# Kernel tuning notes

Measured on AMD Instinct MI355X. Metric: run time of the kernel, lower is better.

## Reference

```python
import jax, jax.numpy as jnp
import numpy as np

B, S, HID, H, D = 4, 1024, 2048, 16, 128
ROT = D // 2  # GLM 2D rotary: rotary dim is half the head dim (64)


def _rope_tables(seq_len, dim, base=10000.0):
    # dim = ROT; inv_freq over dim//2 frequencies, emb = cat(freqs, freqs)
    inv_freq = 1.0 / (base ** (jnp.arange(0, dim, 2, dtype=jnp.float32) / dim))
    t = jnp.arange(seq_len, dtype=jnp.float32)
    freqs = jnp.einsum('s,f->sf', t, inv_freq)          # [S, dim//2]
    emb = jnp.concatenate([freqs, freqs], axis=-1)       # [S, dim]
    return jnp.cos(emb), jnp.sin(emb)


def _rotate_half(x):
    x1, x2 = jnp.split(x, 2, axis=-1)
    return jnp.concatenate([-x2, x1], axis=-1)


def _apply_rope(x, cos, sin, pos_id):
    # x: [B,H,S,ROT]; pos_id: [B,S]; tables: [S,ROT]
    c = cos[pos_id][:, None, :, :]  # [B,1,S,ROT]
    s = sin[pos_id][:, None, :, :]
    return x * c + _rotate_half(x) * s


def setup_inputs() -> dict:
    key = jax.random.key(0)
    ks = jax.random.split(key, 12)
    w = 0.02
    inp = {
        'query': jax.random.normal(ks[0], (B, S, HID), jnp.float32),
        'key': jax.random.normal(ks[1], (B, S, HID), jnp.float32),
        'value': jax.random.normal(ks[2], (B, S, HID), jnp.float32),
        'mask': jnp.zeros((B, 1, S, S), jnp.float32),
        'position_bias': jax.random.normal(ks[3], (1, H, S, S), jnp.float32) * 0.1,
        'prev_attn': jax.random.normal(ks[4], (B, H, S, S), jnp.float32) * 0.1,
        'position_ids': jax.random.randint(ks[5], (B, 2, S), 0, S, jnp.int32),
        'Wq': jax.random.normal(ks[6], (HID, HID), jnp.float32) * w,
        'bq': jnp.zeros((HID,), jnp.float32),
        'Wk': jax.random.normal(ks[7], (HID, HID), jnp.float32) * w,
        'bk': jnp.zeros((HID,), jnp.float32),
        'Wv': jax.random.normal(ks[8], (HID, HID), jnp.float32) * w,
        'bv': jnp.zeros((HID,), jnp.float32),
        'Wo': jax.random.normal(ks[9], (HID, HID), jnp.float32) * w,
        'bo': jnp.zeros((HID,), jnp.float32),
    }
    return inp


def reference(query, key, value, mask, position_bias, prev_attn,
              Wq, bq, Wk, bk, Wv, bv, Wo, bo, position_ids):
    # QKV projections -> [B,H,S,D]
    def proj(x, W, b):
        return (x @ W.T + b).reshape(B, S, H, D).transpose(0, 2, 1, 3)
    q = proj(query, Wq, bq)
    k = proj(key, Wk, bk)
    v = proj(value, Wv, bv)

    # GLM 2D rotary: split head dim in halves, rope each with its own ids
    q1, q2 = jnp.split(q, 2, axis=-1)
    k1, k2 = jnp.split(k, 2, axis=-1)
    cos, sin = _rope_tables(S, ROT)
    pid = position_ids[:, 0, :]        # [B,S]
    bid = position_ids[:, 1, :]        # [B,S]
    q1 = _apply_rope(q1, cos, sin, pid)
    k1 = _apply_rope(k1, cos, sin, pid)
    q2 = _apply_rope(q2, cos, sin, bid)
    k2 = _apply_rope(k2, cos, sin, bid)
    q = jnp.concatenate([q1, q2], axis=-1)
    k = jnp.concatenate([k1, k2], axis=-1)

    scores = jnp.einsum('bhsd,bhtd->bhst', q, k)
    scores = scores + position_bias
    scores = scores / jnp.sqrt(jnp.float32(D))
    scores = scores + mask
    scores = scores + prev_attn          # residual attention accumulation
    prev_attn_out = scores
    probs = jax.nn.softmax(scores, axis=-1)
    ctx = jnp.einsum('bhst,bhtd->bhsd', probs, v)
    ctx = ctx.transpose(0, 2, 1, 3).reshape(B, S, HID)
    out = ctx @ Wo.T + bo
    return out, prev_attn_out
```

## Files before the change

kernel.cpp:

```cpp
#include <hip/hip_runtime.h>


#define B_  4
#define S_  1024
#define HID_ 2048
#define H_  16
#define D_  128
#define M_  (B_ * S_)
#define RSQRT_D 0.08838834764831845f

typedef _Float16 f16x8 __attribute__((ext_vector_type(8)));
typedef float f32x4 __attribute__((ext_vector_type(4)));

#define MFMA16(a, b, c) __builtin_amdgcn_mfma_f32_16x16x32_f16(a, b, c, 0, 0, 0)

__device__ __forceinline__ void gll16(const void* g, void* l) {
  __builtin_amdgcn_global_load_lds(
      (const __attribute__((address_space(1))) void*)g,
      (__attribute__((address_space(3))) void*)l, 16, 0, 0);
}

__global__ void rope_table_kernel(float* __restrict__ tcos, float* __restrict__ tsin) {
  int i = blockIdx.x * blockDim.x + threadIdx.x;
  int pos = i >> 5, j = i & 31;
  float inv = expf(-(float)j * (9.210340371976184f / 32.0f));
  float ang = (float)pos * inv;
  tcos[i] = cosf(ang);
  tsin[i] = sinf(ang);
}

__global__ void cvt_kernel(const float* __restrict__ in, _Float16* __restrict__ out, int n8) {
  int i = blockIdx.x * blockDim.x + threadIdx.x;
  if (i >= n8) return;
  const float4* in4 = (const float4*)in;
  float4 a = in4[i * 2], b = in4[i * 2 + 1];
  f16x8 v;
  v[0] = (_Float16)a.x; v[1] = (_Float16)a.y; v[2] = (_Float16)a.z; v[3] = (_Float16)a.w;
  v[4] = (_Float16)b.x; v[5] = (_Float16)b.y; v[6] = (_Float16)b.z; v[7] = (_Float16)b.w;
  *(f16x8*)(out + (size_t)i * 8) = v;
}

template <int MODE>
__global__ __launch_bounds__(256) void proj_kernel(
    const _Float16* __restrict__ A, const _Float16* __restrict__ Bw,
    const float* __restrict__ bias, void* __restrict__ outp,
    const int* __restrict__ pids, const float* __restrict__ tcos,
    const float* __restrict__ tsin) {
  constexpr int N = HID_, K = HID_;
  constexpr int BK = 64;
  __shared__ _Float16 As[128 * BK];
  __shared__ _Float16 Bs[128 * BK];

  const int tid = threadIdx.x;
  const int bid = (blockIdx.x & 7) * 64 + (blockIdx.x >> 3);
  const int tm = bid >> 4, tn = bid & 15;
  const int m0 = tm * 128, n0 = tn * 128;
  const int w = tid >> 6, l = tid & 63;
  const int mw = (w >> 1) * 64, nw = (w & 1) * 64;
  const int lr = l & 15, lh = l >> 4;

  f32x4 acc[4][4] = {};

  for (int kt = 0; kt < K / BK; ++kt) {
    const int k0 = kt * BK;
    __syncthreads();
#pragma unroll
    for (int i = 0; i < 4; ++i) {
      const int e = i * 2048 + tid * 8;
      gll16(A + (size_t)(m0 + (e >> 6)) * K + k0 + (e & 63), As + e);
      gll16(Bw + (size_t)(n0 + (e >> 6)) * K + k0 + (e & 63), Bs + e);
    }
    asm volatile("s_waitcnt vmcnt(0)" ::: "memory");
    __syncthreads();
#pragma unroll
    for (int kk = 0; kk < 2; ++kk) {
      f16x8 af[4], bf[4];
#pragma unroll
      for (int mi = 0; mi < 4; ++mi)
        af[mi] = *(const f16x8*)(As + (mw + mi * 16 + lr) * BK + kk * 32 + lh * 8);
#pragma unroll
      for (int ni = 0; ni < 4; ++ni)
        bf[ni] = *(const f16x8*)(Bs + (nw + ni * 16 + lr) * BK + kk * 32 + lh * 8);
#pragma unroll
      for (int mi = 0; mi < 4; ++mi)
#pragma unroll
        for (int ni = 0; ni < 4; ++ni)
          acc[mi][ni] = MFMA16(af[mi], bf[ni], acc[mi][ni]);
    }
  }

  if constexpr (MODE == 2) {
    float* out = (float*)outp;
#pragma unroll
    for (int mi = 0; mi < 4; ++mi)
#pragma unroll
      for (int ni = 0; ni < 4; ++ni) {
        const int col = n0 + nw + ni * 16 + lr;
        const float bb = bias[col];
#pragma unroll
        for (int r = 0; r < 4; ++r) {
          const int row = m0 + mw + mi * 16 + lh * 4 + r;
          out[(size_t)row * N + col] = acc[mi][ni][r] + bb;
        }
      }
  } else if constexpr (MODE == 1) {
    _Float16* out = (_Float16*)outp;
#pragma unroll
    for (int mi = 0; mi < 4; ++mi)
#pragma unroll
      for (int ni = 0; ni < 4; ++ni) {
        const int col = n0 + nw + ni * 16 + lr;
        const float bb = bias[col];
        const int h = col >> 7, hd = col & 127;
#pragma unroll
        for (int r = 0; r < 4; ++r) {
          const int row = m0 + mw + mi * 16 + lh * 4 + r;
          const int b = row >> 10, s = row & 1023;
          out[(((size_t)(b * H_ + h)) * S_ + s) * D_ + hd] = (_Float16)(acc[mi][ni][r] + bb);
        }
      }
  } else {
    _Float16* out = (_Float16*)outp;
    const int sel = (nw >> 6) & 1;
#pragma unroll
    for (int mi = 0; mi < 4; ++mi) {
#pragma unroll
      for (int r = 0; r < 4; ++r) {
        const int row = m0 + mw + mi * 16 + lh * 4 + r;
        const int b = row >> 10, s = row & 1023;
        const int pos = pids[b * 2 * S_ + sel * S_ + s];
#pragma unroll
        for (int ni = 0; ni < 2; ++ni) {
          const int col = n0 + nw + ni * 16 + lr;
          const int j = ni * 16 + lr;
          const float c = tcos[pos * 32 + j];
          const float sn = tsin[pos * 32 + j];
          const float x1 = acc[mi][ni][r] + bias[col];
          const float x2 = acc[mi][ni + 2][r] + bias[col + 32];
          const int h = col >> 7, hd = col & 127;
          const size_t base = (((size_t)(b * H_ + h)) * S_ + s) * D_;
          out[base + hd] = (_Float16)(x1 * c - x2 * sn);
          out[base + hd + 32] = (_Float16)(x2 * c + x1 * sn);
        }
      }
    }
  }
}

__global__ __launch_bounds__(256) void transpose_kernel(const _Float16* __restrict__ in,
                                                        _Float16* __restrict__ out) {
  __shared__ _Float16 tile[32][33];
  const int plane = blockIdx.z;
  const int d0 = blockIdx.x * 32, s0 = blockIdx.y * 32;
  const int tx = threadIdx.x & 31, ty = threadIdx.x >> 5;
  const _Float16* ip = in + (size_t)plane * S_ * D_;
  _Float16* op = out + (size_t)plane * S_ * D_;
#pragma unroll
  for (int i = 0; i < 4; ++i)
    tile[ty + i * 8][tx] = ip[(size_t)(s0 + ty + i * 8) * D_ + d0 + tx];
  __syncthreads();
#pragma unroll
  for (int i = 0; i < 4; ++i)
    op[(size_t)(d0 + ty + i * 8) * S_ + s0 + tx] = tile[tx][ty + i * 8];
}

__global__ __launch_bounds__(256) void flash_kernel(
    const _Float16* __restrict__ q, const _Float16* __restrict__ k,
    const _Float16* __restrict__ vt, const float* __restrict__ pbias,
    const float* __restrict__ maskp, const float* __restrict__ prev,
    float* __restrict__ scores, _Float16* __restrict__ ctx) {
  constexpr int BT = 64;
  __shared__ _Float16 Ks[BT * D_];
  __shared__ _Float16 VTs[D_ * BT];
  __shared__ _Float16 Ps[4][16 * BT];

  const int tid = threadIdx.x, w = tid >> 6, l = tid & 63;
  const int lr = l & 15, lh = l >> 4;
  const int byh = blockIdx.y;
  const int b = byh >> 4, h = byh & 15;
  const size_t plane = (size_t)byh;
  const int q0 = blockIdx.x * 64 + w * 16;

  f16x8 qa[4];
#pragma unroll
  for (int kk = 0; kk < 4; ++kk)
    qa[kk] = *(const f16x8*)(q + (plane * S_ + q0 + lr) * D_ + kk * 32 + lh * 8);

  f32x4 o[8] = {};
  float m_r[4], l_r[4];
#pragma unroll
  for (int r = 0; r < 4; ++r) { m_r[r] = -1e30f; l_r[r] = 0.0f; }

  for (int tt = 0; tt < S_ / BT; ++tt) {
    const int t0 = tt * BT;
    __syncthreads();
#pragma unroll
    for (int i = 0; i < 4; ++i) {
      const int e = i * 2048 + tid * 8;
      gll16(k + (plane * S_ + t0 + (e >> 7)) * D_ + (e & 127), Ks + e);
      gll16(vt + (plane * D_ + (e >> 6)) * S_ + t0 + (e & 63), VTs + e);
    }
    asm volatile("s_waitcnt vmcnt(0)" ::: "memory");
    __syncthreads();

    f32x4 sa[4] = {};
#pragma unroll
    for (int nt = 0; nt < 4; ++nt)
#pragma unroll
      for (int kk = 0; kk < 4; ++kk) {
        f16x8 kb = *(const f16x8*)(Ks + (nt * 16 + lr) * D_ + kk * 32 + lh * 8);
        sa[nt] = MFMA16(qa[kk], kb, sa[nt]);
      }

    float p[4][4];
    const int srow_base = q0 + lh * 4;
#pragma unroll
    for (int nt = 0; nt < 4; ++nt) {
      const int t = t0 + nt * 16 + lr;
#pragma unroll
      for (int r = 0; r < 4; ++r) {
        const int srow = srow_base + r;
        const size_t idx = (plane * S_ + srow) * S_ + t;
        float sc = (sa[nt][r] + pbias[((size_t)(h * S_ + srow)) * S_ + t]) * RSQRT_D
                 + maskp[((size_t)(b * S_ + srow)) * S_ + t] + prev[idx];
        scores[idx] = sc;
        p[nt][r] = sc;
      }
    }

#pragma unroll
    for (int r = 0; r < 4; ++r) {
      float tm = fmaxf(fmaxf(p[0][r], p[1][r]), fmaxf(p[2][r], p[3][r]));
      tm = fmaxf(tm, __shfl_xor(tm, 1));
      tm = fmaxf(tm, __shfl_xor(tm, 2));
      tm = fmaxf(tm, __shfl_xor(tm, 4));
      tm = fmaxf(tm, __shfl_xor(tm, 8));
      const float newm = fmaxf(m_r[r], tm);
      const float al = __expf(m_r[r] - newm);
      float ts = 0.0f;
#pragma unroll
      for (int nt = 0; nt < 4; ++nt) { p[nt][r] = __expf(p[nt][r] - newm); ts += p[nt][r]; }
      ts += __shfl_xor(ts, 1);
      ts += __shfl_xor(ts, 2);
      ts += __shfl_xor(ts, 4);
      ts += __shfl_xor(ts, 8);
      l_r[r] = l_r[r] * al + ts;
      m_r[r] = newm;
#pragma unroll
      for (int nd = 0; nd < 8; ++nd) o[nd][r] *= al;
    }

    _Float16* pw = &Ps[w][0];
#pragma unroll
    for (int nt = 0; nt < 4; ++nt)
#pragma unroll
      for (int r = 0; r < 4; ++r)
        pw[(lh * 4 + r) * BT + nt * 16 + lr] = (_Float16)p[nt][r];
    asm volatile("s_waitcnt lgkmcnt(0)" ::: "memory");

#pragma unroll
    for (int kk2 = 0; kk2 < 2; ++kk2) {
      f16x8 pa = *(const f16x8*)(pw + lr * BT + kk2 * 32 + lh * 8);
#pragma unroll
      for (int nd = 0; nd < 8; ++nd) {
        f16x8 vb = *(const f16x8*)(VTs + (nd * 16 + lr) * BT + kk2 * 32 + lh * 8);
        o[nd] = MFMA16(pa, vb, o[nd]);
      }
    }
  }

#pragma unroll
  for (int nd = 0; nd < 8; ++nd) {
    const int d = nd * 16 + lr;
#pragma unroll
    for (int r = 0; r < 4; ++r) {
      const int srow = q0 + lh * 4 + r;
      ctx[((size_t)(b * S_ + srow)) * HID_ + h * D_ + d] = (_Float16)(o[nd][r] / l_r[r]);
    }
  }
}

extern "C" void kernel_launch(void* const* d_in, const int* in_sizes, int n_in,
                              void* d_out, int out_size, void* d_ws, size_t ws_size,
                              hipStream_t stream) {
  const float* query = (const float*)d_in[0];
  const float* key_i = (const float*)d_in[1];
  const float* value = (const float*)d_in[2];
  const float* maskp = (const float*)d_in[3];
  const float* pbias = (const float*)d_in[4];
  const float* prev  = (const float*)d_in[5];
  const int*   pids  = (const int*)d_in[6];
  const float* Wq = (const float*)d_in[7];
  const float* bq = (const float*)d_in[8];
  const float* Wk = (const float*)d_in[9];
  const float* bk = (const float*)d_in[10];
  const float* Wv = (const float*)d_in[11];
  const float* bv = (const float*)d_in[12];
  const float* Wo = (const float*)d_in[13];
  const float* bo = (const float*)d_in[14];

  char* ws = (char*)d_ws;
  const size_t OFF_TCOS = 0;
  const size_t OFF_TSIN = 131072;
  const size_t OFF_W    = 262144;
  const size_t OFF_X    = OFF_W + 4ull * 8388608;
  const size_t OFF_Q    = OFF_X + 3ull * 16777216;
  const size_t OFF_K    = OFF_Q + 16777216;
  const size_t OFF_V    = OFF_K + 16777216;
  const size_t OFF_VT   = OFF_X;
  const size_t OFF_CTX  = OFF_X + 16777216;

  float* tcos = (float*)(ws + OFF_TCOS);
  float* tsin = (float*)(ws + OFF_TSIN);
  _Float16* Wq16 = (_Float16*)(ws + OFF_W);
  _Float16* Wk16 = (_Float16*)(ws + OFF_W + 8388608);
  _Float16* Wv16 = (_Float16*)(ws + OFF_W + 2ull * 8388608);
  _Float16* Wo16 = (_Float16*)(ws + OFF_W + 3ull * 8388608);
  _Float16* Xq16 = (_Float16*)(ws + OFF_X);
  _Float16* Xk16 = (_Float16*)(ws + OFF_X + 16777216);
  _Float16* Xv16 = (_Float16*)(ws + OFF_X + 2ull * 16777216);
  _Float16* q16  = (_Float16*)(ws + OFF_Q);
  _Float16* k16  = (_Float16*)(ws + OFF_K);
  _Float16* v16  = (_Float16*)(ws + OFF_V);
  _Float16* vt16 = (_Float16*)(ws + OFF_VT);
  _Float16* ctx16 = (_Float16*)(ws + OFF_CTX);

  float* out_f32 = (float*)d_out;
  float* scores  = (float*)d_out + 8388608;

  rope_table_kernel<<<128, 256, 0, stream>>>(tcos, tsin);

  cvt_kernel<<<2048, 256, 0, stream>>>(Wq, Wq16, 524288);
  cvt_kernel<<<2048, 256, 0, stream>>>(Wk, Wk16, 524288);
  cvt_kernel<<<2048, 256, 0, stream>>>(Wv, Wv16, 524288);
  cvt_kernel<<<2048, 256, 0, stream>>>(Wo, Wo16, 524288);
  cvt_kernel<<<4096, 256, 0, stream>>>(query, Xq16, 1048576);
  cvt_kernel<<<4096, 256, 0, stream>>>(key_i, Xk16, 1048576);
  cvt_kernel<<<4096, 256, 0, stream>>>(value, Xv16, 1048576);

  proj_kernel<0><<<512, 256, 0, stream>>>(Xq16, Wq16, bq, (void*)q16, pids, tcos, tsin);
  proj_kernel<0><<<512, 256, 0, stream>>>(Xk16, Wk16, bk, (void*)k16, pids, tcos, tsin);
  proj_kernel<1><<<512, 256, 0, stream>>>(Xv16, Wv16, bv, (void*)v16, nullptr, nullptr, nullptr);

  transpose_kernel<<<dim3(4, 32, 64), 256, 0, stream>>>(v16, vt16);

  flash_kernel<<<dim3(16, 64), 256, 0, stream>>>(q16, k16, vt16, pbias, maskp, prev,
                                                 scores, ctx16);

  proj_kernel<2><<<512, 256, 0, stream>>>(ctx16, Wo16, bo, (void*)out_f32,
                                          nullptr, nullptr, nullptr);
}
```

Baseline: 494.8 us.

## Transpose attention MFMA layout for vectorized score I/O and drop V transpose kernel

The V projection epilogue now writes V directly in [B,H,D,S] layout, which removes the separate transpose kernel and its extra buffer pass. The flash kernel swaps the MFMA operands so each lane owns one query row. That lets the fp32 bias, mask, prev_attn reads and the scores writes use 16-byte vector accesses, with nontemporal hints and an early prefetch of prev_attn. It also adds XOR-swizzled LDS layouts to avoid bank conflicts, s_setprio around the MFMA sections, a lazy softmax rescale that only triggers when the row max grows by more than 8, and a 1D block index remapped across XCDs. The changes trade extra index arithmetic for wider memory transactions and fewer kernel launches, and they rely on the rescale threshold keeping fp16 probabilities in range.

```diff
diff --git a/kernel.cpp b/kernel.cpp
--- a/kernel.cpp
+++ b/kernel.cpp
@@ -6,10 +6,10 @@
 #define HID_ 2048
 #define H_  16
 #define D_  128
-#define M_  (B_ * S_)
 #define RSQRT_D 0.08838834764831845f
 
 typedef _Float16 f16x8 __attribute__((ext_vector_type(8)));
+typedef _Float16 f16x4 __attribute__((ext_vector_type(4)));
 typedef float f32x4 __attribute__((ext_vector_type(4)));
 
 #define MFMA16(a, b, c) __builtin_amdgcn_mfma_f32_16x16x32_f16(a, b, c, 0, 0, 0)
@@ -32,11 +32,11 @@
 __global__ void cvt_kernel(const float* __restrict__ in, _Float16* __restrict__ out, int n8) {
   int i = blockIdx.x * blockDim.x + threadIdx.x;
   if (i >= n8) return;
-  const float4* in4 = (const float4*)in;
-  float4 a = in4[i * 2], b = in4[i * 2 + 1];
+  const f32x4* in4 = (const f32x4*)in;
+  f32x4 a = in4[i * 2], b = in4[i * 2 + 1];
   f16x8 v;
-  v[0] = (_Float16)a.x; v[1] = (_Float16)a.y; v[2] = (_Float16)a.z; v[3] = (_Float16)a.w;
-  v[4] = (_Float16)b.x; v[5] = (_Float16)b.y; v[6] = (_Float16)b.z; v[7] = (_Float16)b.w;
+  v[0] = (_Float16)a[0]; v[1] = (_Float16)a[1]; v[2] = (_Float16)a[2]; v[3] = (_Float16)a[3];
+  v[4] = (_Float16)b[0]; v[5] = (_Float16)b[1]; v[6] = (_Float16)b[2]; v[7] = (_Float16)b[3];
   *(f16x8*)(out + (size_t)i * 8) = v;
 }
 
@@ -116,7 +116,7 @@
         for (int r = 0; r < 4; ++r) {
           const int row = m0 + mw + mi * 16 + lh * 4 + r;
           const int b = row >> 10, s = row & 1023;
-          out[(((size_t)(b * H_ + h)) * S_ + s) * D_ + hd] = (_Float16)(acc[mi][ni][r] + bb);
+          out[(((size_t)(b * H_ + h)) * D_ + hd) * S_ + s] = (_Float16)(acc[mi][ni][r] + bb);
         }
       }
   } else {
@@ -147,24 +147,7 @@
   }
 }
 
-__global__ __launch_bounds__(256) void transpose_kernel(const _Float16* __restrict__ in,
-                                                        _Float16* __restrict__ out) {
-  __shared__ _Float16 tile[32][33];
-  const int plane = blockIdx.z;
-  const int d0 = blockIdx.x * 32, s0 = blockIdx.y * 32;
-  const int tx = threadIdx.x & 31, ty = threadIdx.x >> 5;
-  const _Float16* ip = in + (size_t)plane * S_ * D_;
-  _Float16* op = out + (size_t)plane * S_ * D_;
-#pragma unroll
-  for (int i = 0; i < 4; ++i)
-    tile[ty + i * 8][tx] = ip[(size_t)(s0 + ty + i * 8) * D_ + d0 + tx];
-  __syncthreads();
-#pragma unroll
-  for (int i = 0; i < 4; ++i)
-    op[(size_t)(d0 + ty + i * 8) * S_ + s0 + tx] = tile[tx][ty + i * 8];
-}
-
-__global__ __launch_bounds__(256) void flash_kernel(
+__global__ __launch_bounds__(256, 4) void flash_kernel(
     const _Float16* __restrict__ q, const _Float16* __restrict__ k,
     const _Float16* __restrict__ vt, const float* __restrict__ pbias,
     const float* __restrict__ maskp, const float* __restrict__ prev,
@@ -176,20 +159,26 @@
 
   const int tid = threadIdx.x, w = tid >> 6, l = tid & 63;
   const int lr = l & 15, lh = l >> 4;
-  const int byh = blockIdx.y;
+  const int sid = (blockIdx.x & 7) * 128 + (blockIdx.x >> 3);
+  const int qt = sid & 15, byh = sid >> 4;
   const int b = byh >> 4, h = byh & 15;
   const size_t plane = (size_t)byh;
-  const int q0 = blockIdx.x * 64 + w * 16;
+  const int q0 = qt * 64 + w * 16;
+  const int qrow = q0 + lr;
+  const int swz = (lr & 7) << 3;
+
+  const float* prow  = prev  + (plane * S_ + qrow) * S_;
+  const float* pbrow = pbias + ((size_t)h * S_ + qrow) * S_;
+  const float* mrow  = maskp + ((size_t)b * S_ + qrow) * S_;
+  float*       srow  = scores + (plane * S_ + qrow) * S_;
 
   f16x8 qa[4];
 #pragma unroll
   for (int kk = 0; kk < 4; ++kk)
-    qa[kk] = *(const f16x8*)(q + (plane * S_ + q0 + lr) * D_ + kk * 32 + lh * 8);
+    qa[kk] = *(const f16x8*)(q + (plane * S_ + qrow) * D_ + kk * 32 + lh * 8);
 
   f32x4 o[8] = {};
-  float m_r[4], l_r[4];
-#pragma unroll
-  for (int r = 0; r < 4; ++r) { m_r[r] = -1e30f; l_r[r] = 0.0f; }
+  float m_r = -1e30f, l_r = 0.0f;
 
   for (int tt = 0; tt < S_ / BT; ++tt) {
     const int t0 = tt * BT;
@@ -197,86 +186,99 @@
 #pragma unroll
     for (int i = 0; i < 4; ++i) {
       const int e = i * 2048 + tid * 8;
-      gll16(k + (plane * S_ + t0 + (e >> 7)) * D_ + (e & 127), Ks + e);
-      gll16(vt + (plane * D_ + (e >> 6)) * S_ + t0 + (e & 63), VTs + e);
-    }
+      const int krow = e >> 7;
+      gll16(k + (plane * S_ + t0 + krow) * D_ + ((e & 127) ^ ((krow & 7) << 3)), Ks + e);
+      const int vrow = e >> 6;
+      gll16(vt + (plane * D_ + vrow) * S_ + t0 + ((e & 63) ^ ((vrow & 7) << 3)), VTs + e);
+    }
+    f32x4 pv4[4];
+#pragma unroll
+    for (int nt = 0; nt < 4; ++nt)
+      pv4[nt] = __builtin_nontemporal_load((const f32x4*)(prow + t0 + nt * 16 + lh * 4));
     asm volatile("s_waitcnt vmcnt(0)" ::: "memory");
     __syncthreads();
 
     f32x4 sa[4] = {};
+    __builtin_amdgcn_s_setprio(1);
 #pragma unroll
     for (int nt = 0; nt < 4; ++nt)
 #pragma unroll
       for (int kk = 0; kk < 4; ++kk) {
-        f16x8 kb = *(const f16x8*)(Ks + (nt * 16 + lr) * D_ + kk * 32 + lh * 8);
-        sa[nt] = MFMA16(qa[kk], kb, sa[nt]);
-      }
-
-    float p[4][4];
-    const int srow_base = q0 + lh * 4;
+        const int row = nt * 16 + lr;
+        f16x8 kb = *(const f16x8*)(Ks + row * D_ + ((kk * 32 + lh * 8) ^ swz));
+        sa[nt] = MFMA16(kb, qa[kk], sa[nt]);
+      }
+    __builtin_amdgcn_s_setprio(0);
+
 #pragma unroll
     for (int nt = 0; nt < 4; ++nt) {
-      const int t = t0 + nt * 16 + lr;
+      const int toff = t0 + nt * 16 + lh * 4;
+      const f32x4 pb4 = *(const f32x4*)(pbrow + toff);
+      const f32x4 mk4 = *(const f32x4*)(mrow + toff);
+      f32x4 sc4 = (sa[nt] + pb4) * RSQRT_D + mk4 + pv4[nt];
+      __builtin_nontemporal_store(sc4, (f32x4*)(srow + toff));
+      sa[nt] = sc4;
+    }
+
+    float tmx = -1e30f;
+#pragma unroll
+    for (int nt = 0; nt < 4; ++nt)
+#pragma unroll
+      for (int r = 0; r < 4; ++r) tmx = fmaxf(tmx, sa[nt][r]);
+    tmx = fmaxf(tmx, __shfl_xor(tmx, 16));
+    tmx = fmaxf(tmx, __shfl_xor(tmx, 32));
+    if (!__all(tmx <= m_r + 8.0f)) {
+      const float newm = fmaxf(m_r, tmx);
+      const float al = __expf(m_r - newm);
+      m_r = newm;
+      l_r *= al;
+#pragma unroll
+      for (int nd = 0; nd < 8; ++nd) o[nd] *= al;
+    }
+    float ts = 0.0f;
+#pragma unroll
+    for (int nt = 0; nt < 4; ++nt)
 #pragma unroll
       for (int r = 0; r < 4; ++r) {
-        const int srow = srow_base + r;
-        const size_t idx = (plane * S_ + srow) * S_ + t;
-        float sc = (sa[nt][r] + pbias[((size_t)(h * S_ + srow)) * S_ + t]) * RSQRT_D
-                 + maskp[((size_t)(b * S_ + srow)) * S_ + t] + prev[idx];
-        scores[idx] = sc;
-        p[nt][r] = sc;
-      }
-    }
-
-#pragma unroll
-    for (int r = 0; r < 4; ++r) {
-      float tm = fmaxf(fmaxf(p[0][r], p[1][r]), fmaxf(p[2][r], p[3][r]));
-      tm = fmaxf(tm, __shfl_xor(tm, 1));
-      tm = fmaxf(tm, __shfl_xor(tm, 2));
-      tm = fmaxf(tm, __shfl_xor(tm, 4));
-      tm = fmaxf(tm, __shfl_xor(tm, 8));
-      const float newm = fmaxf(m_r[r], tm);
-      const float al = __expf(m_r[r] - newm);
-      float ts = 0.0f;
-#pragma unroll
-      for (int nt = 0; nt < 4; ++nt) { p[nt][r] = __expf(p[nt][r] - newm); ts += p[nt][r]; }
-      ts += __shfl_xor(ts, 1);
-      ts += __shfl_xor(ts, 2);
-      ts += __shfl_xor(ts, 4);
-      ts += __shfl_xor(ts, 8);
-      l_r[r] = l_r[r] * al + ts;
-      m_r[r] = newm;
-#pragma unroll
-      for (int nd = 0; nd < 8; ++nd) o[nd][r] *= al;
-    }
+        const float pe = __expf(sa[nt][r] - m_r);
+        sa[nt][r] = pe;
+        ts += pe;
+      }
+    ts += __shfl_xor(ts, 16);
+    ts += __shfl_xor(ts, 32);
+    l_r += ts;
 
     _Float16* pw = &Ps[w][0];
 #pragma unroll
-    for (int nt = 0; nt < 4; ++nt)
-#pragma unroll
-      for (int r = 0; r < 4; ++r)
-        pw[(lh * 4 + r) * BT + nt * 16 + lr] = (_Float16)p[nt][r];
-    asm volatile("s_waitcnt lgkmcnt(0)" ::: "memory");
-
-#pragma unroll
-    for (int kk2 = 0; kk2 < 2; ++kk2) {
-      f16x8 pa = *(const f16x8*)(pw + lr * BT + kk2 * 32 + lh * 8);
+    for (int nt = 0; nt < 4; ++nt) {
+      f16x4 pk;
+      pk[0] = (_Float16)sa[nt][0]; pk[1] = (_Float16)sa[nt][1];
+      pk[2] = (_Float16)sa[nt][2]; pk[3] = (_Float16)sa[nt][3];
+      *(f16x4*)(pw + lr * BT + ((nt * 16 + lh * 4) ^ swz)) = pk;
+    }
+
+    __builtin_amdgcn_s_setprio(1);
+#pragma unroll
+    for (int kk = 0; kk < 2; ++kk) {
+      const f16x8 pa = *(const f16x8*)(pw + lr * BT + ((kk * 32 + lh * 8) ^ swz));
 #pragma unroll
       for (int nd = 0; nd < 8; ++nd) {
-        f16x8 vb = *(const f16x8*)(VTs + (nd * 16 + lr) * BT + kk2 * 32 + lh * 8);
-        o[nd] = MFMA16(pa, vb, o[nd]);
-      }
-    }
+        const int vr = nd * 16 + lr;
+        const f16x8 vb = *(const f16x8*)(VTs + vr * BT + ((kk * 32 + lh * 8) ^ swz));
+        o[nd] = MFMA16(vb, pa, o[nd]);
+      }
+    }
+    __builtin_amdgcn_s_setprio(0);
   }
 
+  const float inv_l = 1.0f / l_r;
+  _Float16* crow = ctx + ((size_t)(b * S_) + qrow) * HID_ + h * D_;
 #pragma unroll
   for (int nd = 0; nd < 8; ++nd) {
-    const int d = nd * 16 + lr;
-#pragma unroll
-    for (int r = 0; r < 4; ++r) {
-      const int srow = q0 + lh * 4 + r;
-      ctx[((size_t)(b * S_ + srow)) * HID_ + h * D_ + d] = (_Float16)(o[nd][r] / l_r[r]);
-    }
+    f16x4 cv;
+#pragma unroll
+    for (int r = 0; r < 4; ++r) cv[r] = (_Float16)(o[nd][r] * inv_l);
+    *(f16x4*)(crow + nd * 16 + lh * 4) = cv;
   }
 }
 
@@ -306,8 +308,7 @@
   const size_t OFF_X    = OFF_W + 4ull * 8388608;
   const size_t OFF_Q    = OFF_X + 3ull * 16777216;
   const size_t OFF_K    = OFF_Q + 16777216;
-  const size_t OFF_V    = OFF_K + 16777216;
-  const size_t OFF_VT   = OFF_X;
+  const size_t OFF_VT   = OFF_K + 16777216;
   const size_t OFF_CTX  = OFF_X + 16777216;
 
   float* tcos = (float*)(ws + OFF_TCOS);
@@ -321,7 +322,6 @@
   _Float16* Xv16 = (_Float16*)(ws + OFF_X + 2ull * 16777216);
   _Float16* q16  = (_Float16*)(ws + OFF_Q);
   _Float16* k16  = (_Float16*)(ws + OFF_K);
-  _Float16* v16  = (_Float16*)(ws + OFF_V);
   _Float16* vt16 = (_Float16*)(ws + OFF_VT);
   _Float16* ctx16 = (_Float16*)(ws + OFF_CTX);
 
@@ -340,12 +340,10 @@
 
   proj_kernel<0><<<512, 256, 0, stream>>>(Xq16, Wq16, bq, (void*)q16, pids, tcos, tsin);
   proj_kernel<0><<<512, 256, 0, stream>>>(Xk16, Wk16, bk, (void*)k16, pids, tcos, tsin);
-  proj_kernel<1><<<512, 256, 0, stream>>>(Xv16, Wv16, bv, (void*)v16, nullptr, nullptr, nullptr);
-
-  transpose_kernel<<<dim3(4, 32, 64), 256, 0, stream>>>(v16, vt16);
-
-  flash_kernel<<<dim3(16, 64), 256, 0, stream>>>(q16, k16, vt16, pbias, maskp, prev,
-                                                 scores, ctx16);
+  proj_kernel<1><<<512, 256, 0, stream>>>(Xv16, Wv16, bv, (void*)vt16, nullptr, nullptr, nullptr);
+
+  flash_kernel<<<1024, 256, 0, stream>>>(q16, k16, vt16, pbias, maskp, prev,
+                                         scores, ctx16);
 
   proj_kernel<2><<<512, 256, 0, stream>>>(ctx16, Wo16, bo, (void*)out_f32,
                                           nullptr, nullptr, nullptr);
```

Measured after the change: 512.5 us. 1.04x slower.
